# Kernel optimization log

Measured on AMD Instinct MI355X. Metric: run time of the kernel, lower is better.

The kernel has to match this reference:

```python
import jax, jax.numpy as jnp
import numpy as np

EPS = 1e-6


def setup_inputs() -> dict:
    key = jax.random.key(0)
    ks = jax.random.split(key, 8)
    B, L, C = 2, 512, 768  # d_model=768, C//3=256
    pairDim = 128
    inp = {
        "x": jax.random.normal(ks[0], (B, L, C), dtype=jnp.float32),
        "ln_w": jnp.ones((C,), jnp.float32),
        "ln_b": jnp.zeros((C,), jnp.float32),
        # torch Linear weights are [out, in]
        "W1": jax.random.normal(ks[1], (256, C // 3), jnp.float32) * (1.0 / np.sqrt(C // 3)),
        "b1": jax.random.normal(ks[2], (256,), jnp.float32) * 0.02,
        "Wa": jax.random.normal(ks[3], (64, 64), jnp.float32) * (1.0 / np.sqrt(64)),
        "ba": jax.random.normal(ks[4], (64,), jnp.float32) * 0.02,
        "W2": jax.random.normal(ks[5], (pairDim, 32), jnp.float32) * (1.0 / np.sqrt(32)),
        "b2": jax.random.normal(ks[6], (pairDim,), jnp.float32) * 0.02,
    }
    return inp


def _layernorm(x, w, b):
    mu = jnp.mean(x, axis=-1, keepdims=True)
    var = jnp.mean(jnp.square(x - mu), axis=-1, keepdims=True)
    return (x - mu) * jax.lax.rsqrt(var + EPS) * w + b


def reference(x, ln_w, ln_b, W1, b1, Wa, ba, W2, b2):
    B, L, C = x.shape
    h = _layernorm(x, ln_w, ln_b)                      # [B,L,C]
    h = h.reshape(B, L, 3, C // 3)                     # [B,L,3,C/3]
    t = (h @ W1.T + b1).reshape(B, L, 3, 32, 8)        # [B,L,3,32,8]
    # outer product t[...,i]*t[...,j] then mean over the 3 chunks (fused)
    mean_out = jnp.einsum('blkci,blkcj->blcij', t, t) / 3.0  # [B,L,32,8,8]
    mean_out = mean_out.reshape(B, L, 32, 64).transpose(0, 2, 1, 3)  # [B,32,L,64]
    mean_trans = jax.nn.gelu(mean_out @ Wa.T + ba, approximate=False)  # [B,32,L,64]
    raw = jnp.einsum('bcld,bcmd->bclm', mean_out, mean_trans)  # [B,32,L,L]
    raw = raw.transpose(0, 2, 3, 1)                    # [B,L,L,32]
    return raw @ W2.T + b2                             # [B,L,L,pairDim]
```

## Files before the change

kernel.cpp:

```cpp
#include <hip/hip_runtime.h>
#include <math.h>


typedef __attribute__((ext_vector_type(8))) _Float16 half8;
typedef __attribute__((ext_vector_type(4))) _Float16 half4;
typedef __attribute__((ext_vector_type(4))) float f32x4;

#define MFMA_F16(a,b,c) __builtin_amdgcn_mfma_f32_16x16x32_f16((a),(b),(c),0,0,0)

static __device__ inline unsigned pack2f16(float a, float b) {
    _Float16 ha = (_Float16)a, hb = (_Float16)b;
    unsigned short ua = __builtin_bit_cast(unsigned short, ha);
    unsigned short ub = __builtin_bit_cast(unsigned short, hb);
    return (unsigned)ua | ((unsigned)ub << 16);
}

static __device__ inline half8 cvt8(float4 u, float4 v) {
    half8 h;
    h[0] = (_Float16)u.x; h[1] = (_Float16)u.y; h[2] = (_Float16)u.z; h[3] = (_Float16)u.w;
    h[4] = (_Float16)v.x; h[5] = (_Float16)v.y; h[6] = (_Float16)v.z; h[7] = (_Float16)v.w;
    return h;
}

__global__ __launch_bounds__(256) void k0_pack(const float* __restrict__ W1, _Float16* __restrict__ W1H)
{
    int flat8 = blockIdx.x * 256 + threadIdx.x;
    int j  = flat8 >> 5, i8 = flat8 & 31;
    int nt = j >> 4, lr = j & 15, ks = i8 >> 2, lk = i8 & 3;
    const float4* src = (const float4*)(W1 + (size_t)j * 256 + (size_t)i8 * 8);
    half8 h = cvt8(src[0], src[1]);
    *(half8*)(W1H + (((size_t)(nt * 8 + ks) * 64) + lk * 16 + lr) * 8) = h;
}

__global__ __launch_bounds__(256) void k1_rowstage(
    const float* __restrict__ x, const float* __restrict__ ln_w, const float* __restrict__ ln_b,
    const _Float16* __restrict__ W1H, const float* __restrict__ b1,
    const float* __restrict__ Wa, const float* __restrict__ ba,
    _Float16* __restrict__ mo_g, _Float16* __restrict__ mt_g)
{
    const int bl  = blockIdx.x;
    const int tid = threadIdx.x;
    const int b   = bl >> 9;
    const int l   = bl & 511;
    const int w   = tid >> 6;
    const int lane = tid & 63;
    const int lr  = lane & 15;
    const int lk  = lane >> 4;

    __shared__ _Float16 hs16[4 * 272];
    __shared__ float ts[768];
    __shared__ float mos[32 * 68];
    __shared__ float ws1[4], ws2[4];

    const float* xrow = x + (size_t)bl * 768;
    float v0 = xrow[tid], v1 = xrow[tid + 256], v2 = xrow[tid + 512];

    half8 waf[2];
    #pragma unroll
    for (int ks = 0; ks < 2; ++ks) {
        const float* wp = Wa + (size_t)(w * 16 + lr) * 64 + ks * 32 + lk * 8;
        waf[ks] = cvt8(*(const float4*)wp, *(const float4*)(wp + 4));
    }
    const float4 baq = *(const float4*)(ba + w * 16 + lk * 4);

    float s1 = v0 + v1 + v2;
    float s2 = v0 * v0 + v1 * v1 + v2 * v2;
    #pragma unroll
    for (int off = 32; off > 0; off >>= 1) {
        s1 += __shfl_down(s1, off);
        s2 += __shfl_down(s2, off);
    }
    if ((tid & 63) == 0) { ws1[tid >> 6] = s1; ws2[tid >> 6] = s2; }
    __syncthreads();
    float tot1 = ws1[0] + ws1[1] + ws1[2] + ws1[3];
    float tot2 = ws2[0] + ws2[1] + ws2[2] + ws2[3];
    float mu   = tot1 * (1.0f / 768.0f);
    float var  = tot2 * (1.0f / 768.0f) - mu * mu;
    float rstd = rsqrtf(var + 1e-6f);

    hs16[tid]            = (_Float16)((v0 - mu) * rstd * ln_w[tid]       + ln_b[tid]);
    hs16[272 + tid]      = (_Float16)((v1 - mu) * rstd * ln_w[tid + 256] + ln_b[tid + 256]);
    hs16[544 + tid]      = (_Float16)((v2 - mu) * rstd * ln_w[tid + 512] + ln_b[tid + 512]);
    hs16[816 + tid]      = (_Float16)0.0f;
    __syncthreads();

    {
        f32x4 acc[4] = {};
        #pragma unroll
        for (int ks = 0; ks < 8; ++ks) {
            half8 af = *(const half8*)&hs16[(lr & 3) * 272 + ks * 32 + lk * 8];
            #pragma unroll
            for (int n = 0; n < 4; ++n) {
                half8 bf = *(const half8*)(W1H + (((size_t)((w * 4 + n) * 8 + ks) * 64) + lane) * 8);
                acc[n] = MFMA_F16(af, bf, acc[n]);
            }
        }
        if (lk == 0) {
            #pragma unroll
            for (int n = 0; n < 4; ++n) {
                int j = (w * 4 + n) * 16 + lr;
                float bb = b1[j];
                ts[j]       = acc[n][0] + bb;
                ts[256 + j] = acc[n][1] + bb;
                ts[512 + j] = acc[n][2] + bb;
            }
        }
    }
    __syncthreads();

    {
        const int c = tid >> 3, i = tid & 7;
        float ti0 = ts[c * 8 + i], ti1 = ts[256 + c * 8 + i], ti2 = ts[512 + c * 8 + i];
        half8 h8;
        #pragma unroll
        for (int j = 0; j < 8; j++) {
            float m = (ti0 * ts[c * 8 + j] + ti1 * ts[256 + c * 8 + j] + ti2 * ts[512 + c * 8 + j]) * (1.0f / 3.0f);
            mos[c * 68 + i * 8 + j] = m;
            h8[j] = (_Float16)m;
        }
        size_t mobase = ((size_t)(b * 32 + c) * 512 + l) * 64 + i * 8;
        *(half8*)(mo_g + mobase) = h8;
    }
    __syncthreads();

    #pragma unroll
    for (int nt = 0; nt < 2; ++nt) {
        f32x4 acc = { baq.x, baq.y, baq.z, baq.w };
        #pragma unroll
        for (int ks = 0; ks < 2; ++ks) {
            const float* mp = &mos[(nt * 16 + lr) * 68 + ks * 32 + lk * 8];
            half8 mof = cvt8(*(const float4*)mp, *(const float4*)(mp + 4));
            acc = MFMA_F16(waf[ks], mof, acc);
        }
        half4 o;
        #pragma unroll
        for (int j = 0; j < 4; ++j) {
            float g = 0.5f * acc[j] * (1.0f + erff(acc[j] * 0.70710678118654752f));
            o[j] = (_Float16)g;
        }
        *(half4*)(mt_g + ((size_t)(b * 32 + nt * 16 + lr) * 512 + l) * 64 + w * 16 + lk * 4) = o;
    }
}

__global__ __launch_bounds__(256, 2) void k2_mfma(
    const _Float16* __restrict__ mo, const _Float16* __restrict__ mt,
    const float* __restrict__ W2, const float* __restrict__ b2,
    float* __restrict__ out)
{
    __shared__ _Float16 raw16[512 * 40];
    __shared__ float sc[4][2048];

    const int tid  = threadIdx.x;
    const int w    = tid >> 6;
    const int lane = tid & 63;
    const int lr   = lane & 15;
    const int lk   = lane >> 4;

    const int flat = blockIdx.x;
    const int nf   = (flat & 7) * 128 + (flat >> 3);
    const int m0   = (nf & 31) << 4;
    const int l0   = ((nf >> 5) & 15) << 5;
    const int b    = nf >> 9;

    #pragma unroll
    for (int cp = 0; cp < 4; ++cp) {
        const int c0 = w * 8 + cp * 2;
        f32x4 acc[2][2] = {};
        #pragma unroll
        for (int ci = 0; ci < 2; ++ci) {
            const int c = c0 + ci;
            const _Float16* mo_c = mo + (((size_t)(b * 32 + c) * 512) + l0) * 64;
            const _Float16* mt_c = mt + (((size_t)(b * 32 + c) * 512) + m0) * 64;
            #pragma unroll
            for (int ks = 0; ks < 2; ++ks) {
                half8 bfrag = *(const half8*)(mt_c + (size_t)lr * 64 + ks * 32 + lk * 8);
                #pragma unroll
                for (int rh = 0; rh < 2; ++rh) {
                    half8 afrag = *(const half8*)(mo_c + (size_t)(rh * 16 + lr) * 64 + ks * 32 + lk * 8);
                    acc[ci][rh] = MFMA_F16(afrag, bfrag, acc[ci][rh]);
                }
            }
        }
        #pragma unroll
        for (int rh = 0; rh < 2; ++rh) {
            #pragma unroll
            for (int j = 0; j < 4; ++j) {
                int pair = (rh * 16 + lk * 4 + j) * 16 + lr;
                int sw   = (((pair >> 3) & 1) << 3) | (((pair >> 6) & 1) << 4);
                *(unsigned*)&raw16[pair * 40 + (c0 ^ sw)] = pack2f16(acc[0][rh][j], acc[1][rh][j]);
            }
        }
    }

    half8 wfrag[8]; float4 b2q[8];
    #pragma unroll
    for (int c8 = 0; c8 < 8; ++c8) {
        const float* wp = W2 + (size_t)(c8 * 16 + lr) * 32 + lk * 8;
        wfrag[c8] = cvt8(*(const float4*)wp, *(const float4*)(wp + 4));
        b2q[c8]   = *(const float4*)(b2 + c8 * 16 + lk * 4);
    }
    __syncthreads();

    for (int i = 0; i < 8; ++i) {
        const int r  = w * 8 + i;
        const int pr = r * 16 + lr;
        const int swr = (((pr >> 3) & 1) << 3) | (((pr >> 6) & 1) << 4);
        half8 a = *(const half8*)&raw16[pr * 40 + ((lk * 8) ^ swr)];

        #pragma unroll
        for (int c8 = 0; c8 < 8; ++c8) {
            f32x4 d = { b2q[c8].x, b2q[c8].y, b2q[c8].z, b2q[c8].w };
            d = MFMA_F16(wfrag[c8], a, d);
            int chunk = (c8 * 4 + lk) ^ lr;
            *(f32x4*)&sc[w][lr * 128 + chunk * 4] = d;
        }
        float* ob = out + (((size_t)(b * 512 + l0 + r)) * 512 + m0) * 128;
        #pragma unroll
        for (int s = 0; s < 8; ++s) {
            int mm = s * 2 + (lane >> 5);
            int cp = (lane & 31) ^ mm;
            f32x4 v = *(const f32x4*)&sc[w][mm * 128 + cp * 4];
            __builtin_nontemporal_store(v, (f32x4*)(ob + s * 256 + lane * 4));
        }
    }
}

extern "C" void kernel_launch(void* const* d_in, const int* in_sizes, int n_in,
                              void* d_out, int out_size, void* d_ws, size_t ws_size,
                              hipStream_t stream) {
    const float* x    = (const float*)d_in[0];
    const float* ln_w = (const float*)d_in[1];
    const float* ln_b = (const float*)d_in[2];
    const float* W1   = (const float*)d_in[3];
    const float* b1   = (const float*)d_in[4];
    const float* Wa   = (const float*)d_in[5];
    const float* ba   = (const float*)d_in[6];
    const float* W2   = (const float*)d_in[7];
    const float* b2   = (const float*)d_in[8];
    float* out = (float*)d_out;

    _Float16* mo  = (_Float16*)d_ws;
    _Float16* mt  = mo + (size_t)2 * 32 * 512 * 64;
    _Float16* W1H = mt + (size_t)2 * 32 * 512 * 64;

    k0_pack<<<32, 256, 0, stream>>>(W1, W1H);
    k1_rowstage<<<1024, 256, 0, stream>>>(x, ln_w, ln_b, W1H, b1, Wa, ba, mo, mt);
    k2_mfma<<<1024, 256, 0, stream>>>(mo, mt, W2, b2, out);
}
```

Baseline: 78.22 us.

## Process four rows per block in row-stage kernel to fill MFMA tiles

The row-stage kernel now handles four sequence positions per block instead of one, so the 16-row MFMA A-tile holds 12 real rows (4 positions × 3 chunks) rather than 3, and each W1 fragment load is amortised across four rows. LayerNorm is done per-wave with float4 loads and xor-shuffle reductions, which removes the cross-wave shared-memory reduction and one barrier. The grid shrinks from 1024 to 256 blocks and shared memory per block grows, which lowers parallelism and may reduce occupancy. The per-thread outer-product and GELU loops grow fourfold.

```diff
diff --git a/kernel.cpp b/kernel.cpp
--- a/kernel.cpp
+++ b/kernel.cpp
@@ -32,28 +32,24 @@
     *(half8*)(W1H + (((size_t)(nt * 8 + ks) * 64) + lk * 16 + lr) * 8) = h;
 }
 
-__global__ __launch_bounds__(256) void k1_rowstage(
+__global__ __launch_bounds__(256) void k1_rowstage4(
     const float* __restrict__ x, const float* __restrict__ ln_w, const float* __restrict__ ln_b,
     const _Float16* __restrict__ W1H, const float* __restrict__ b1,
     const float* __restrict__ Wa, const float* __restrict__ ba,
     _Float16* __restrict__ mo_g, _Float16* __restrict__ mt_g)
 {
-    const int bl  = blockIdx.x;
+    const int blk = blockIdx.x;
+    const int b   = blk >> 7;
+    const int l0  = (blk & 127) << 2;
     const int tid = threadIdx.x;
-    const int b   = bl >> 9;
-    const int l   = bl & 511;
     const int w   = tid >> 6;
     const int lane = tid & 63;
     const int lr  = lane & 15;
     const int lk  = lane >> 4;
 
-    __shared__ _Float16 hs16[4 * 272];
-    __shared__ float ts[768];
-    __shared__ float mos[32 * 68];
-    __shared__ float ws1[4], ws2[4];
-
-    const float* xrow = x + (size_t)bl * 768;
-    float v0 = xrow[tid], v1 = xrow[tid + 256], v2 = xrow[tid + 512];
+    __shared__ _Float16 hs16[16 * 280];
+    __shared__ float ts4[4][776];
+    __shared__ float mos4[4][2176];
 
     half8 waf[2];
     #pragma unroll
@@ -63,46 +59,61 @@
     }
     const float4 baq = *(const float4*)(ba + w * 16 + lk * 4);
 
-    float s1 = v0 + v1 + v2;
-    float s2 = v0 * v0 + v1 * v1 + v2 * v2;
-    #pragma unroll
-    for (int off = 32; off > 0; off >>= 1) {
-        s1 += __shfl_down(s1, off);
-        s2 += __shfl_down(s2, off);
-    }
-    if ((tid & 63) == 0) { ws1[tid >> 6] = s1; ws2[tid >> 6] = s2; }
-    __syncthreads();
-    float tot1 = ws1[0] + ws1[1] + ws1[2] + ws1[3];
-    float tot2 = ws2[0] + ws2[1] + ws2[2] + ws2[3];
-    float mu   = tot1 * (1.0f / 768.0f);
-    float var  = tot2 * (1.0f / 768.0f) - mu * mu;
-    float rstd = rsqrtf(var + 1e-6f);
-
-    hs16[tid]            = (_Float16)((v0 - mu) * rstd * ln_w[tid]       + ln_b[tid]);
-    hs16[272 + tid]      = (_Float16)((v1 - mu) * rstd * ln_w[tid + 256] + ln_b[tid + 256]);
-    hs16[544 + tid]      = (_Float16)((v2 - mu) * rstd * ln_w[tid + 512] + ln_b[tid + 512]);
-    hs16[816 + tid]      = (_Float16)0.0f;
+    {
+        const float4* xrow = (const float4*)(x + ((size_t)(b * 512 + l0 + w)) * 768);
+        float4 xv[3];
+        float s1 = 0.f, s2 = 0.f;
+        #pragma unroll
+        for (int e4 = 0; e4 < 3; ++e4) {
+            float4 v = xrow[lane + 64 * e4];
+            xv[e4] = v;
+            s1 += v.x + v.y + v.z + v.w;
+            s2 += v.x * v.x + v.y * v.y + v.z * v.z + v.w * v.w;
+        }
+        #pragma unroll
+        for (int off = 32; off > 0; off >>= 1) {
+            s1 += __shfl_xor(s1, off);
+            s2 += __shfl_xor(s2, off);
+        }
+        float mu   = s1 * (1.0f / 768.0f);
+        float var  = s2 * (1.0f / 768.0f) - mu * mu;
+        float rstd = rsqrtf(var + 1e-6f);
+        #pragma unroll
+        for (int e4 = 0; e4 < 3; ++e4) {
+            float4 lw = ((const float4*)ln_w)[lane + 64 * e4];
+            float4 lb = ((const float4*)ln_b)[lane + 64 * e4];
+            half4 h4;
+            h4[0] = (_Float16)((xv[e4].x - mu) * rstd * lw.x + lb.x);
+            h4[1] = (_Float16)((xv[e4].y - mu) * rstd * lw.y + lb.y);
+            h4[2] = (_Float16)((xv[e4].z - mu) * rstd * lw.z + lb.z);
+            h4[3] = (_Float16)((xv[e4].w - mu) * rstd * lw.w + lb.w);
+            *(half4*)&hs16[(w * 3 + e4) * 280 + 4 * lane] = h4;
+        }
+    }
     __syncthreads();
 
     {
         f32x4 acc[4] = {};
         #pragma unroll
         for (int ks = 0; ks < 8; ++ks) {
-            half8 af = *(const half8*)&hs16[(lr & 3) * 272 + ks * 32 + lk * 8];
+            half8 af = *(const half8*)&hs16[lr * 280 + ks * 32 + lk * 8];
             #pragma unroll
             for (int n = 0; n < 4; ++n) {
                 half8 bf = *(const half8*)(W1H + (((size_t)((w * 4 + n) * 8 + ks) * 64) + lane) * 8);
                 acc[n] = MFMA_F16(af, bf, acc[n]);
             }
         }
-        if (lk == 0) {
-            #pragma unroll
-            for (int n = 0; n < 4; ++n) {
-                int j = (w * 4 + n) * 16 + lr;
-                float bb = b1[j];
-                ts[j]       = acc[n][0] + bb;
-                ts[256 + j] = acc[n][1] + bb;
-                ts[512 + j] = acc[n][2] + bb;
+        #pragma unroll
+        for (int n = 0; n < 4; ++n) {
+            int j = (w * 4 + n) * 16 + lr;
+            float bb = b1[j];
+            #pragma unroll
+            for (int jj = 0; jj < 4; ++jj) {
+                int m = lk * 4 + jj;
+                if (m < 12) {
+                    int r = m / 3, k = m - r * 3;
+                    ts4[r][k * 256 + j] = acc[n][jj] + bb;
+                }
             }
         }
     }
@@ -110,25 +121,30 @@
 
     {
         const int c = tid >> 3, i = tid & 7;
-        float ti0 = ts[c * 8 + i], ti1 = ts[256 + c * 8 + i], ti2 = ts[512 + c * 8 + i];
-        half8 h8;
-        #pragma unroll
-        for (int j = 0; j < 8; j++) {
-            float m = (ti0 * ts[c * 8 + j] + ti1 * ts[256 + c * 8 + j] + ti2 * ts[512 + c * 8 + j]) * (1.0f / 3.0f);
-            mos[c * 68 + i * 8 + j] = m;
-            h8[j] = (_Float16)m;
-        }
-        size_t mobase = ((size_t)(b * 32 + c) * 512 + l) * 64 + i * 8;
-        *(half8*)(mo_g + mobase) = h8;
-    }
-    __syncthreads();
-
-    #pragma unroll
-    for (int nt = 0; nt < 2; ++nt) {
+        #pragma unroll
+        for (int r = 0; r < 4; ++r) {
+            float ti0 = ts4[r][c * 8 + i], ti1 = ts4[r][256 + c * 8 + i], ti2 = ts4[r][512 + c * 8 + i];
+            half8 h8;
+            #pragma unroll
+            for (int j = 0; j < 8; j++) {
+                float m = (ti0 * ts4[r][c * 8 + j] + ti1 * ts4[r][256 + c * 8 + j]
+                         + ti2 * ts4[r][512 + c * 8 + j]) * (1.0f / 3.0f);
+                mos4[r][c * 68 + i * 8 + j] = m;
+                h8[j] = (_Float16)m;
+            }
+            size_t mobase = ((size_t)(b * 32 + c) * 512 + (l0 + r)) * 64 + i * 8;
+            *(half8*)(mo_g + mobase) = h8;
+        }
+    }
+    __syncthreads();
+
+    #pragma unroll
+    for (int nt2 = 0; nt2 < 8; ++nt2) {
+        const int r = nt2 >> 1, ch = nt2 & 1;
         f32x4 acc = { baq.x, baq.y, baq.z, baq.w };
         #pragma unroll
         for (int ks = 0; ks < 2; ++ks) {
-            const float* mp = &mos[(nt * 16 + lr) * 68 + ks * 32 + lk * 8];
+            const float* mp = &mos4[r][(ch * 16 + lr) * 68 + ks * 32 + lk * 8];
             half8 mof = cvt8(*(const float4*)mp, *(const float4*)(mp + 4));
             acc = MFMA_F16(waf[ks], mof, acc);
         }
@@ -138,7 +154,7 @@
             float g = 0.5f * acc[j] * (1.0f + erff(acc[j] * 0.70710678118654752f));
             o[j] = (_Float16)g;
         }
-        *(half4*)(mt_g + ((size_t)(b * 32 + nt * 16 + lr) * 512 + l) * 64 + w * 16 + lk * 4) = o;
+        *(half4*)(mt_g + ((size_t)(b * 32 + ch * 16 + lr) * 512 + (l0 + r)) * 64 + w * 16 + lk * 4) = o;
     }
 }
 
@@ -244,6 +260,6 @@
     _Float16* W1H = mt + (size_t)2 * 32 * 512 * 64;
 
     k0_pack<<<32, 256, 0, stream>>>(W1, W1H);
-    k1_rowstage<<<1024, 256, 0, stream>>>(x, ln_w, ln_b, W1H, b1, Wa, ba, mo, mt);
+    k1_rowstage4<<<256, 256, 0, stream>>>(x, ln_w, ln_b, W1H, b1, Wa, ba, mo, mt);
     k2_mfma<<<1024, 256, 0, stream>>>(mo, mt, W2, b2, out);
 }
```

New measurement: 77.26 us. Within noise of the previous version (-1.2%).
